# Kernel optimization log

Measured on AMD Instinct MI355X. Metric: run time of the kernel, lower is better.

The kernel has to match this reference:

```python
import jax, jax.numpy as jnp
import numpy as np

B, F, N_P, N_Q, DIM, H = 16, 16, 196, 32, 768, 12

def setup_inputs() -> dict:
    key = jax.random.key(0)
    ks = jax.random.split(key, 6)
    return {
        "x": jax.random.normal(ks[0], (B, F * N_P, DIM), jnp.float32),
        "question": jax.random.normal(ks[1], (B, N_Q, DIM), jnp.float32),
        "Wq": jax.random.normal(ks[2], (DIM, DIM), jnp.float32) * 0.02,
        "Wkv": jax.random.normal(ks[3], (DIM, 2 * DIM), jnp.float32) * 0.02,
        "Wproj": jax.random.normal(ks[4], (DIM, DIM), jnp.float32) * 0.02,
        "bproj": jnp.zeros((DIM,), jnp.float32),
        "mask": jnp.zeros((B, F * N_P), jnp.bool_),
        "whether": 0,
        "f": F,
    }

def reference(x, question, Wq, Wkv, Wproj, bproj, mask, whether, f):
    # mask and whether are unused by the original forward as well
    num_heads = H
    b, n_kv, dim = x.shape
    n_q = question.shape[1]
    d = dim // num_heads
    scale = d ** -0.5
    # projections; split heads: b n (h d) -> b h n d
    q = (question @ Wq).reshape(b, n_q, num_heads, d).transpose(0, 2, 1, 3) * scale
    k, v = jnp.split(x @ Wkv, 2, axis=-1)
    k = k.reshape(b, n_kv, num_heads, d).transpose(0, 2, 1, 3)
    v = v.reshape(b, n_kv, num_heads, d).transpose(0, 2, 1, 3)
    cls_q = q[:, :, :1]   # b h 1 d  -- CLS attends over all video tokens
    q_ = q[:, :, 1:]      # b h (n_q-1) d -- rest attend per-frame
    cls_sim = jnp.einsum('bhid,bhjd->bhij', cls_q, k)
    cls_out = jnp.einsum('bhij,bhjd->bhid', jax.nn.softmax(cls_sim, axis=-1), v)
    n_p = n_kv // f
    kf = k.reshape(b, num_heads, f, n_p, d)
    vf = v.reshape(b, num_heads, f, n_p, d)
    # q_ broadcast across frames == repeat_interleave(f, 0) in the original
    sim = jnp.einsum('bhid,bhfjd->bhfij', q_, kf)
    out = jnp.einsum('bhfij,bhfjd->bhfid', jax.nn.softmax(sim, axis=-1), vf)
    # '(b f) n d -> b (f n) d' with frame-major ordering
    out = out.reshape(b, num_heads, f * (n_q - 1), d)
    out = jnp.concatenate([cls_out, out], axis=2)  # b h (1 + f*(n_q-1)) d
    out = out.transpose(0, 2, 1, 3).reshape(b, 1 + f * (n_q - 1), dim)
    return out @ Wproj + bproj
```

## Files before the change

kernel.cpp:

```cpp
#include <hip/hip_runtime.h>

typedef unsigned short u16;
typedef __bf16 bf16x8 __attribute__((ext_vector_type(8)));
typedef float f32x4 __attribute__((ext_vector_type(4)));

__device__ __forceinline__ u16 f2bf(float f) {
  union { float f; unsigned u; } v; v.f = f;
  unsigned r = (v.u + 0x7FFFu + ((v.u >> 16) & 1u)) >> 16;
  return (u16)r;
}
__device__ __forceinline__ float bf2f(u16 u) {
  union { unsigned u; float f; } v; v.u = ((unsigned)u) << 16;
  return v.f;
}

#define GLD16(g, l) __builtin_amdgcn_global_load_lds((const __attribute__((address_space(1))) void*)(g), (__attribute__((address_space(3))) void*)(l), 16, 0, 0)
#define LOG2E 1.44269504f

__global__ __launch_bounds__(256) void mega_prep(const float* __restrict__ x, u16* __restrict__ xb,
                                                 int have_xb,
                                                 const float* __restrict__ Wq, u16* __restrict__ WqT,
                                                 const float* __restrict__ Wkv, u16* __restrict__ WkvT,
                                                 const float* __restrict__ Wproj, u16* __restrict__ WprojT) {
  __shared__ float t[32][33];
  int bid = blockIdx.x;
  if (bid < 2048) {
    if (!have_xb) return;
    const size_t n8 = (size_t)50176 * 768 / 8;
    const size_t stride = (size_t)2048 * 256;
    for (size_t i = (size_t)bid * 256 + threadIdx.x; i < n8; i += stride) {
      float4 a = *(const float4*)(x + i * 8);
      float4 b = *(const float4*)(x + i * 8 + 4);
      ushort4 oa, ob;
      oa.x = f2bf(a.x); oa.y = f2bf(a.y); oa.z = f2bf(a.z); oa.w = f2bf(a.w);
      ob.x = f2bf(b.x); ob.y = f2bf(b.y); ob.z = f2bf(b.z); ob.w = f2bf(b.w);
      ushort4* o = (ushort4*)(xb + i * 8);
      o[0] = oa; o[1] = ob;
    }
    return;
  }
  bid -= 2048;
  const float* in; u16* outp; int N;
  const int K = 768;
  if (bid < 576) { in = Wq; outp = WqT; N = 768; }
  else if (bid < 1728) { in = Wkv; outp = WkvT; N = 1536; bid -= 576; }
  else { in = Wproj; outp = WprojT; N = 768; bid -= 1728; }
  int nb = N >> 5;
  int bn = bid % nb, bk = bid / nb;
  int tx = threadIdx.x & 31, ty = threadIdx.x >> 5;
#pragma unroll
  for (int i = 0; i < 4; ++i)
    t[ty + i * 8][tx] = in[(size_t)(bk * 32 + ty + i * 8) * N + bn * 32 + tx];
  __syncthreads();
#pragma unroll
  for (int i = 0; i < 4; ++i)
    outp[(size_t)(bn * 32 + ty + i * 8) * K + bk * 32 + tx] = f2bf(t[tx][ty + i * 8]);
}

__global__ __launch_bounds__(512, 2) void gemm256_bt(const u16* __restrict__ A,
                                                     const u16* __restrict__ Bt,
                                                     u16* __restrict__ C,
                                                     int M, int N) {
  __shared__ __align__(16) char smem[131072];
  const int KB = 1536;
  int nb = N >> 8;
  int nwg = gridDim.x;
  int bid = blockIdx.x;
  if (!(nwg & 7)) { int cpx = nwg >> 3; bid = (bid & 7) * cpx + (bid >> 3); }
  int bm = bid / nb, bn = bid - bm * nb;
  int tid = threadIdx.x, lane = tid & 63, wid = tid >> 6;
  int wm = wid >> 2, wn = wid & 3;
  int l15 = lane & 15, g4 = lane >> 4;

  int goff[4][2], loff[4][2];
#pragma unroll
  for (int p = 0; p < 4; ++p) {
#pragma unroll
    for (int i = 0; i < 2; ++i) {
      int idx = wid * 2 + i;
      int ht = p & 1;
      int base;
      if (p < 2) base = ht * 8192 + (idx >> 3) * 16384 + (idx & 7) * 1024;
      else       base = (idx >> 2) * 8192 + ht * 4096 + (idx & 3) * 1024;
      int pb = base + 16 * lane;
      int lb = pb ^ (((pb >> 9) & 1) << 5);
      goff[p][i] = (lb >> 7) * KB + (lb & 127);
      loff[p][i] = pb;
    }
  }
  const char* Agb = (const char*)A + (size_t)bm * 256 * KB;
  const char* Bgb = (const char*)Bt + (size_t)bn * 256 * KB;

  auto STAGE = [&](int pat, int buf, int k0) {
    const char* gb = (pat < 2) ? Agb : Bgb;
    int lbase = buf * 65536 + ((pat < 2) ? 0 : 32768);
#pragma unroll
    for (int i = 0; i < 2; ++i)
      GLD16(gb + goff[pat][i] + k0 * 2, smem + lbase + loff[pat][i]);
  };

  f32x4 acc[8][4];
  const f32x4 fz = {0.f, 0.f, 0.f, 0.f};
#pragma unroll
  for (int a = 0; a < 8; ++a)
#pragma unroll
    for (int b = 0; b < 4; ++b) acc[a][b] = fz;
  bf16x8 af[4][2], bv[2][2];

  auto RDA = [&](int buf, int qm) {
#pragma unroll
    for (int mi = 0; mi < 4; ++mi)
#pragma unroll
      for (int ks = 0; ks < 2; ++ks) {
        int lb = (wm * 128 + qm * 64 + mi * 16 + l15) * 128 + ks * 64 + g4 * 16;
        int pb = lb ^ (((lb >> 9) & 1) << 5);
        af[mi][ks] = *(const bf16x8*)(smem + buf * 65536 + pb);
      }
  };
  auto RDB = [&](int buf, int qn) {
#pragma unroll
    for (int ni = 0; ni < 2; ++ni)
#pragma unroll
      for (int ks = 0; ks < 2; ++ks) {
        int lb = (wn * 64 + qn * 32 + ni * 16 + l15) * 128 + ks * 64 + g4 * 16;
        int pb = lb ^ (((lb >> 9) & 1) << 5);
        bv[ni][ks] = *(const bf16x8*)(smem + buf * 65536 + 32768 + pb);
      }
  };
  auto MM = [&](int qm, int qn) {
    __builtin_amdgcn_s_setprio(1);
#pragma unroll
    for (int mi = 0; mi < 4; ++mi)
#pragma unroll
      for (int ni = 0; ni < 2; ++ni)
#pragma unroll
        for (int ks = 0; ks < 2; ++ks)
          acc[qm * 4 + mi][qn * 2 + ni] =
              __builtin_amdgcn_mfma_f32_16x16x32_bf16(af[mi][ks], bv[ni][ks],
                                                      acc[qm * 4 + mi][qn * 2 + ni], 0, 0, 0);
    __builtin_amdgcn_s_setprio(0);
  };
#define BAR() __builtin_amdgcn_s_barrier()
#define LGKM0() asm volatile("s_waitcnt lgkmcnt(0)" ::: "memory")

  STAGE(0, 0, 0); STAGE(2, 0, 0); STAGE(1, 0, 0); STAGE(3, 0, 0);
  STAGE(0, 1, 64); STAGE(2, 1, 64);
  asm volatile("s_waitcnt vmcnt(4)" ::: "memory");
  BAR();

  for (int t = 0; t < 6; ++t) {
    int kO = t * 128 + 64, kE2 = t * 128 + 128, kO2 = t * 128 + 192;
    bool lst = (t == 5);
    RDA(0, 0); RDB(0, 0); STAGE(1, 1, kO);
    BAR(); LGKM0(); MM(0, 0); BAR();
    RDB(0, 1); STAGE(3, 1, kO);
    BAR(); LGKM0(); MM(0, 1); BAR();
    RDA(0, 1); RDB(0, 0); if (!lst) STAGE(0, 0, kE2);
    BAR(); LGKM0(); MM(1, 0); BAR();
    RDB(0, 1); if (!lst) STAGE(2, 0, kE2);
    BAR(); LGKM0(); MM(1, 1);
    if (lst) asm volatile("s_waitcnt vmcnt(0)" ::: "memory");
    else     asm volatile("s_waitcnt vmcnt(4)" ::: "memory");
    BAR();
    RDA(1, 0); RDB(1, 0); if (!lst) STAGE(1, 0, kE2);
    BAR(); LGKM0(); MM(0, 0); BAR();
    RDB(1, 1); if (!lst) STAGE(3, 0, kE2);
    BAR(); LGKM0(); MM(0, 1); BAR();
    RDA(1, 1); RDB(1, 0); if (!lst) STAGE(0, 1, kO2);
    BAR(); LGKM0(); MM(1, 0); BAR();
    RDB(1, 1); if (!lst) STAGE(2, 1, kO2);
    BAR(); LGKM0(); MM(1, 1);
    if (!lst) asm volatile("s_waitcnt vmcnt(4)" ::: "memory");
    BAR();
  }
#undef BAR
#undef LGKM0

#pragma unroll
  for (int a = 0; a < 8; ++a)
#pragma unroll
    for (int b = 0; b < 4; ++b)
#pragma unroll
      for (int r = 0; r < 4; ++r)
        C[(size_t)(bm * 256 + wm * 128 + a * 16 + g4 * 4 + r) * N + bn * 256 + wn * 64 + b * 16 + l15] =
            f2bf(acc[a][b][r]);
}

template <int AF32, int OUTF32>
__global__ __launch_bounds__(256) void gemm_bt(const void* __restrict__ Av,
                                               const u16* __restrict__ Bt,
                                               void* __restrict__ Cv,
                                               const float* __restrict__ bias,
                                               float scale, int M, int N, int K) {
  __shared__ u16 As[128 * 32];
  __shared__ u16 Bs[128 * 32];
  int nb = N >> 7;
  int nwg = gridDim.x;
  int bid = blockIdx.x;
  if (!(nwg & 7)) { int cpx = nwg >> 3; bid = (bid & 7) * cpx + (bid >> 3); }
  int bm = bid / nb, bn = bid - bm * nb;
  int tid = threadIdx.x, lane = tid & 63, w = tid >> 6;
  int wr = w >> 1, wc = w & 1;
  int l15 = lane & 15, g4 = lane >> 4;

  const f32x4 fz = {0.f, 0.f, 0.f, 0.f};
  f32x4 acc[4][4];
#pragma unroll
  for (int m = 0; m < 4; ++m)
#pragma unroll
    for (int n = 0; n < 4; ++n) acc[m][n] = fz;

  const int kIters = K >> 5;
  for (int kt = 0; kt < kIters; ++kt) {
    __syncthreads();
    const int k0 = kt << 5;
    if constexpr (AF32) {
      const float* Af = (const float*)Av;
#pragma unroll
      for (int i = 0; i < 4; ++i) {
        int c = tid + (i << 8);
        int row = c >> 3, cp = c & 7;
        int grow = bm * 128 + row; if (grow > M - 1) grow = M - 1;
        float4 v = *(const float4*)(Af + (size_t)grow * K + k0 + cp * 4);
        ushort4 o; o.x = f2bf(v.x); o.y = f2bf(v.y); o.z = f2bf(v.z); o.w = f2bf(v.w);
        *(ushort4*)&As[row * 32 + cp * 4] = o;
      }
    } else {
      const u16* Ab = (const u16*)Av;
#pragma unroll
      for (int i = 0; i < 2; ++i) {
        int c = tid + (i << 8);
        int row = c >> 2, cp = c & 3;
        int grow = bm * 128 + row; if (grow > M - 1) grow = M - 1;
        GLD16(Ab + (size_t)grow * K + k0 + cp * 8, &As[row * 32 + cp * 8]);
      }
    }
#pragma unroll
    for (int i = 0; i < 2; ++i) {
      int c = tid + (i << 8);
      int row = c >> 2, cp = c & 3;
      GLD16(Bt + (size_t)(bn * 128 + row) * K + k0 + cp * 8, &Bs[row * 32 + cp * 8]);
    }
    __syncthreads();
    bf16x8 af[4], bfr[4];
#pragma unroll
    for (int m = 0; m < 4; ++m)
      af[m] = *(const bf16x8*)&As[(wr * 64 + m * 16 + l15) * 32 + g4 * 8];
#pragma unroll
    for (int n = 0; n < 4; ++n)
      bfr[n] = *(const bf16x8*)&Bs[(wc * 64 + n * 16 + l15) * 32 + g4 * 8];
#pragma unroll
    for (int m = 0; m < 4; ++m)
#pragma unroll
      for (int n = 0; n < 4; ++n)
        acc[m][n] = __builtin_amdgcn_mfma_f32_16x16x32_bf16(af[m], bfr[n], acc[m][n], 0, 0, 0);
  }
  int r0 = bm * 128 + wr * 64;
  int c0 = bn * 128 + wc * 64;
#pragma unroll
  for (int m = 0; m < 4; ++m) {
#pragma unroll
    for (int n = 0; n < 4; ++n) {
      int col = c0 + n * 16 + l15;
      float badd = bias ? bias[col] : 0.f;
#pragma unroll
      for (int r = 0; r < 4; ++r) {
        int grow = r0 + m * 16 + g4 * 4 + r;
        if (grow < M) {
          float v = acc[m][n][r] * scale + badd;
          if constexpr (OUTF32) ((float*)Cv)[(size_t)grow * N + col] = v;
          else ((u16*)Cv)[(size_t)grow * N + col] = f2bf(v);
        }
      }
    }
  }
}

#define CLS_CH 16
__global__ __launch_bounds__(64) void cls_reduce(const float* __restrict__ part,
                                                 u16* __restrict__ ATT) {
  int bh = blockIdx.x;
  int b = bh / 12, h = bh % 12;
  int d = threadIdx.x;
  float m[CLS_CH], l[CLS_CH];
  float M = -1e30f;
#pragma unroll
  for (int c = 0; c < CLS_CH; ++c) {
    m[c] = part[(size_t)(bh * CLS_CH + c) * 66 + 64];
    l[c] = part[(size_t)(bh * CLS_CH + c) * 66 + 65];
    M = fmaxf(M, m[c]);
  }
  float L = 0.f, o = 0.f;
#pragma unroll
  for (int c = 0; c < CLS_CH; ++c) {
    float wgt = exp2f((m[c] - M) * LOG2E) * l[c];
    L += wgt;
    o += wgt * part[(size_t)(bh * CLS_CH + c) * 66 + d];
  }
  ATT[(size_t)(b * 497) * 768 + h * 64 + d] = f2bf(o / L);
}

#define VSTR 232
__global__ __launch_bounds__(256, 3) void frame_attn(const u16* __restrict__ Qp,
                                                     const u16* __restrict__ KV,
                                                     u16* __restrict__ ATT,
                                                     float* __restrict__ part) {
  __shared__ u16 Vt[64 * VSTR];
  __shared__ u16 P[32 * VSTR];
  __shared__ float redm[2][32];
  __shared__ float reds[2][32];

  int bid = blockIdx.x;
  int b = bid / 192;
  int h = (bid / 16) % 12;
  int f = bid % 16;
  int tid = threadIdx.x, lane = tid & 63, w = tid >> 6;
  int l15 = lane & 15, g4 = lane >> 4;
  int mt = w >> 1, nh = w & 1;

  const u16* Kb = KV + ((size_t)(b * 3136 + f * 196)) * 1536 + h * 64;
  const u16* Vb = Kb + 768;
  const u16* Qbp = Qp + (size_t)(b * 32) * 768 + h * 64;

  int qrow = mt * 16 + l15;
  bf16x8 qf[2];
  qf[0] = *(const bf16x8*)(Qbp + (size_t)qrow * 768 + g4 * 8);
  qf[1] = *(const bf16x8*)(Qbp + (size_t)qrow * 768 + 32 + g4 * 8);

  bf16x8 kfa[7][2];
#pragma unroll
  for (int nt = 0; nt < 7; ++nt) {
    if (!(nh == 1 && nt == 6)) {
      int j = nh * 112 + nt * 16 + l15;
      kfa[nt][0] = *(const bf16x8*)(Kb + (size_t)j * 1536 + g4 * 8);
      kfa[nt][1] = *(const bf16x8*)(Kb + (size_t)j * 1536 + 32 + g4 * 8);
    }
  }

  int vd8 = tid & 7;
  int vr0 = (tid >> 3) * 2;
  uint4 va[3][2];
#pragma unroll
  for (int i = 0; i < 3; ++i) {
    int j = vr0 + i * 64;
    va[i][0] = *(const uint4*)(Vb + (size_t)j * 1536 + vd8 * 8);
    va[i][1] = *(const uint4*)(Vb + (size_t)(j + 1) * 1536 + vd8 * 8);
  }
  bool vtail = (vr0 < 4);
  uint4 vt0, vt1;
  if (vtail) {
    vt0 = *(const uint4*)(Vb + (size_t)(vr0 + 192) * 1536 + vd8 * 8);
    vt1 = *(const uint4*)(Vb + (size_t)(vr0 + 193) * 1536 + vd8 * 8);
  }
  for (int c = tid; c < 64 * 28; c += 256) {
    int d = c / 28, j = 196 + (c - d * 28);
    Vt[d * VSTR + j] = 0;
  }

  const f32x4 fz = {0.f, 0.f, 0.f, 0.f};
  f32x4 s[7];
#pragma unroll
  for (int i = 0; i < 7; ++i) s[i] = fz;
#pragma unroll
  for (int nt = 0; nt < 7; ++nt) {
    if (!(nh == 1 && nt == 6)) {
      s[nt] = __builtin_amdgcn_mfma_f32_16x16x32_bf16(qf[0], kfa[nt][0], s[nt], 0, 0, 0);
      s[nt] = __builtin_amdgcn_mfma_f32_16x16x32_bf16(qf[1], kfa[nt][1], s[nt], 0, 0, 0);
    }
  }
  const f32x4 fneg = {-1e30f, -1e30f, -1e30f, -1e30f};
#pragma unroll
  for (int nt = 0; nt < 7; ++nt) {
    int j = nh * 112 + nt * 16 + l15;
    if (j >= 196) s[nt] = fneg;
  }
  float pm[4], psum[4];
#pragma unroll
  for (int r = 0; r < 4; ++r) {
    float m = s[0][r];
#pragma unroll
    for (int nt = 1; nt < 7; ++nt) m = fmaxf(m, s[nt][r]);
    m = fmaxf(m, __shfl_xor(m, 1));
    m = fmaxf(m, __shfl_xor(m, 2));
    m = fmaxf(m, __shfl_xor(m, 4));
    m = fmaxf(m, __shfl_xor(m, 8));
    pm[r] = m;
    psum[r] = 0.f;
  }
#pragma unroll
  for (int nt = 0; nt < 7; ++nt)
#pragma unroll
    for (int r = 0; r < 4; ++r) {
      float e = exp2f((s[nt][r] - pm[r]) * LOG2E);
      s[nt][r] = e;
      psum[r] += e;
    }
#pragma unroll
  for (int r = 0; r < 4; ++r) {
    psum[r] += __shfl_xor(psum[r], 1);
    psum[r] += __shfl_xor(psum[r], 2);
    psum[r] += __shfl_xor(psum[r], 4);
    psum[r] += __shfl_xor(psum[r], 8);
  }
  if (l15 == 0) {
#pragma unroll
    for (int r = 0; r < 4; ++r) {
      redm[nh][mt * 16 + g4 * 4 + r] = pm[r];
      reds[nh][mt * 16 + g4 * 4 + r] = psum[r];
    }
  }
  __syncthreads();

#pragma unroll
  for (int i = 0; i < 3; ++i) {
    const u16* a = (const u16*)&va[i][0];
    const u16* bq = (const u16*)&va[i][1];
    int j = vr0 + i * 64;
#pragma unroll
    for (int e = 0; e < 8; ++e) {
      unsigned wv = (unsigned)a[e] | ((unsigned)bq[e] << 16);
      *(unsigned*)&Vt[(vd8 * 8 + e) * VSTR + j] = wv;
    }
  }
  if (vtail) {
    const u16* a = (const u16*)&vt0;
    const u16* bq = (const u16*)&vt1;
    int j = vr0 + 192;
#pragma unroll
    for (int e = 0; e < 8; ++e) {
      unsigned wv = (unsigned)a[e] | ((unsigned)bq[e] << 16);
      *(unsigned*)&Vt[(vd8 * 8 + e) * VSTR + j] = wv;
    }
  }

  float M0 = 0.f, L0 = 1.f;
#pragma unroll
  for (int r = 0; r < 4; ++r) {
    int row = mt * 16 + g4 * 4 + r;
    float m0 = redm[0][row], m1 = redm[1][row];
    float M = fmaxf(m0, m1);
    float L = reds[0][row] * exp2f((m0 - M) * LOG2E) + reds[1][row] * exp2f((m1 - M) * LOG2E);
    if (r == 0) { M0 = M; L0 = L; }
    float fac = exp2f((pm[r] - M) * LOG2E) / L;
#pragma unroll
    for (int nt = 0; nt < 7; ++nt)
      P[row * VSTR + nh * 112 + nt * 16 + l15] = f2bf(s[nt][r] * fac);
  }
  __syncthreads();

  f32x4 o0 = fz, o1 = fz;
  int prow = mt * 16 + l15;
#pragma unroll
  for (int ks = 0; ks < 7; ++ks) {
    bf16x8 pa = *(const bf16x8*)&P[prow * VSTR + ks * 32 + g4 * 8];
    bf16x8 v0 = *(const bf16x8*)&Vt[(nh * 32 + l15) * VSTR + ks * 32 + g4 * 8];
    bf16x8 v1 = *(const bf16x8*)&Vt[(nh * 32 + 16 + l15) * VSTR + ks * 32 + g4 * 8];
    o0 = __builtin_amdgcn_mfma_f32_16x16x32_bf16(pa, v0, o0, 0, 0, 0);
    o1 = __builtin_amdgcn_mfma_f32_16x16x32_bf16(pa, v1, o1, 0, 0, 0);
  }
  u16* Ab = ATT + ((size_t)b * 497) * 768 + h * 64;
#pragma unroll
  for (int r = 0; r < 4; ++r) {
    int qi = mt * 16 + g4 * 4 + r;
    if (qi > 0) {
      size_t ro = (size_t)(f * 31 + qi) * 768;
      Ab[ro + nh * 32 + l15] = f2bf(o0[r]);
      Ab[ro + nh * 32 + 16 + l15] = f2bf(o1[r]);
    }
  }
  if (mt == 0 && g4 == 0) {
    float* po = part + (size_t)(((b * 12 + h) * 16) + f) * 66;
    po[nh * 32 + l15] = o0[0];
    po[nh * 32 + 16 + l15] = o1[0];
    if (nh == 0 && l15 == 0) { po[64] = M0; po[65] = L0; }
  }
}

extern "C" void kernel_launch(void* const* d_in, const int* in_sizes, int n_in,
                              void* d_out, int out_size, void* d_ws, size_t ws_size,
                              hipStream_t stream) {
  const float* x = (const float*)d_in[0];
  const float* question = (const float*)d_in[1];
  const float* Wq = (const float*)d_in[2];
  const float* Wkv = (const float*)d_in[3];
  const float* Wproj = (const float*)d_in[4];
  const float* bproj = (const float*)d_in[5];
  float* out = (float*)d_out;

  char* ws = (char*)d_ws;
  size_t off = 0;
  auto carve = [&](size_t elems) {
    u16* p = (u16*)(ws + off);
    off += ((elems * 2 + 255) & ~(size_t)255);
    return p;
  };
  u16* WqT = carve((size_t)768 * 768);
  u16* WkvT = carve((size_t)1536 * 768);
  u16* WprojT = carve((size_t)768 * 768);
  u16* Qb = carve((size_t)512 * 768);
  u16* KV = carve((size_t)50176 * 1536);
  u16* ATT = carve((size_t)7952 * 768);
  float* PART = (float*)carve((size_t)192 * CLS_CH * 66 * 2);
  size_t base_need = off;
  u16* xb = carve((size_t)50176 * 768);
  if (ws_size < base_need) return;
  int have_xb = (ws_size >= off) ? 1 : 0;

  mega_prep<<<2048 + 576 + 1152 + 576, 256, 0, stream>>>(x, xb, have_xb,
                                                         Wq, WqT, Wkv, WkvT, Wproj, WprojT);
  gemm_bt<1, 0><<<4 * 6, 256, 0, stream>>>(question, WqT, Qb, nullptr, 0.125f, 512, 768, 768);
  if (have_xb) {
    gemm256_bt<<<196 * 6, 512, 0, stream>>>(xb, WkvT, KV, 50176, 1536);
  } else {
    gemm_bt<1, 0><<<392 * 12, 256, 0, stream>>>(x, WkvT, KV, nullptr, 1.0f, 50176, 1536, 768);
  }
  frame_attn<<<3072, 256, 0, stream>>>(Qb, KV, ATT, PART);
  cls_reduce<<<192, 64, 0, stream>>>(PART, ATT);
  gemm_bt<0, 1><<<63 * 6, 256, 0, stream>>>(ATT, WprojT, out, bproj, 1.0f, 7952, 768, 768);
}
```

Baseline: 305.1 us.

## Fuse fp32-to-bf16 conversion of x into the KV projection GEMM

```diff
diff --git a/kernel.cpp b/kernel.cpp
--- a/kernel.cpp
+++ b/kernel.cpp
@@ -17,29 +17,11 @@
 #define GLD16(g, l) __builtin_amdgcn_global_load_lds((const __attribute__((address_space(1))) void*)(g), (__attribute__((address_space(3))) void*)(l), 16, 0, 0)
 #define LOG2E 1.44269504f
 
-__global__ __launch_bounds__(256) void mega_prep(const float* __restrict__ x, u16* __restrict__ xb,
-                                                 int have_xb,
-                                                 const float* __restrict__ Wq, u16* __restrict__ WqT,
+__global__ __launch_bounds__(256) void mega_prep(const float* __restrict__ Wq, u16* __restrict__ WqT,
                                                  const float* __restrict__ Wkv, u16* __restrict__ WkvT,
                                                  const float* __restrict__ Wproj, u16* __restrict__ WprojT) {
   __shared__ float t[32][33];
   int bid = blockIdx.x;
-  if (bid < 2048) {
-    if (!have_xb) return;
-    const size_t n8 = (size_t)50176 * 768 / 8;
-    const size_t stride = (size_t)2048 * 256;
-    for (size_t i = (size_t)bid * 256 + threadIdx.x; i < n8; i += stride) {
-      float4 a = *(const float4*)(x + i * 8);
-      float4 b = *(const float4*)(x + i * 8 + 4);
-      ushort4 oa, ob;
-      oa.x = f2bf(a.x); oa.y = f2bf(a.y); oa.z = f2bf(a.z); oa.w = f2bf(a.w);
-      ob.x = f2bf(b.x); ob.y = f2bf(b.y); ob.z = f2bf(b.z); ob.w = f2bf(b.w);
-      ushort4* o = (ushort4*)(xb + i * 8);
-      o[0] = oa; o[1] = ob;
-    }
-    return;
-  }
-  bid -= 2048;
   const float* in; u16* outp; int N;
   const int K = 768;
   if (bid < 576) { in = Wq; outp = WqT; N = 768; }
@@ -57,11 +39,12 @@
     outp[(size_t)(bn * 32 + ty + i * 8) * K + bk * 32 + tx] = f2bf(t[tx][ty + i * 8]);
 }
 
-__global__ __launch_bounds__(512, 2) void gemm256_bt(const u16* __restrict__ A,
+__global__ __launch_bounds__(512, 2) void gemm256_ax(const float* __restrict__ Af,
                                                      const u16* __restrict__ Bt,
                                                      u16* __restrict__ C,
                                                      int M, int N) {
   __shared__ __align__(16) char smem[131072];
+  const int KBf = 3072;
   const int KB = 1536;
   int nb = N >> 8;
   int nwg = gridDim.x;
@@ -72,7 +55,7 @@
   int wm = wid >> 2, wn = wid & 3;
   int l15 = lane & 15, g4 = lane >> 4;
 
-  int goff[4][2], loff[4][2];
+  int ga32[2][2], gb[2][2], loffA[2][2], loffB[2][2];
 #pragma unroll
   for (int p = 0; p < 4; ++p) {
 #pragma unroll
@@ -84,19 +67,41 @@
       else       base = (idx >> 2) * 8192 + ht * 4096 + (idx & 3) * 1024;
       int pb = base + 16 * lane;
       int lb = pb ^ (((pb >> 9) & 1) << 5);
-      goff[p][i] = (lb >> 7) * KB + (lb & 127);
-      loff[p][i] = pb;
-    }
-  }
-  const char* Agb = (const char*)A + (size_t)bm * 256 * KB;
+      if (p < 2) { ga32[p][i] = (lb >> 7) * KBf + (lb & 127) * 2; loffA[p][i] = pb; }
+      else       { gb[p - 2][i] = (lb >> 7) * KB + (lb & 127);    loffB[p - 2][i] = pb; }
+    }
+  }
+  const char* Agb = (const char*)Af + (size_t)bm * 256 * KBf;
   const char* Bgb = (const char*)Bt + (size_t)bn * 256 * KB;
 
-  auto STAGE = [&](int pat, int buf, int k0) {
-    const char* gb = (pat < 2) ? Agb : Bgb;
-    int lbase = buf * 65536 + ((pat < 2) ? 0 : 32768);
+  float4 ar[2][2];
+  auto LDA = [&](int pat, int k0) {
+#pragma unroll
+    for (int i = 0; i < 2; ++i) {
+      const char* s = Agb + ga32[pat][i] + k0 * 4;
+      ar[i][0] = *(const float4*)(s);
+      ar[i][1] = *(const float4*)(s + 16);
+    }
+  };
+  auto WRA = [&](int pat, int buf) {
+#pragma unroll
+    for (int i = 0; i < 2; ++i) {
+      union { u16 h[8]; uint4 v; } r;
+      const float* f0 = (const float*)&ar[i][0];
+      const float* f1 = (const float*)&ar[i][1];
+#pragma unroll
+      for (int e = 0; e < 4; ++e) {
+        union { __bf16 b; u16 u; } c0; c0.b = (__bf16)f0[e]; r.h[e] = c0.u;
+        union { __bf16 b; u16 u; } c1; c1.b = (__bf16)f1[e]; r.h[4 + e] = c1.u;
+      }
+      *(uint4*)(smem + buf * 65536 + loffA[pat][i]) = r.v;
+    }
+  };
+  auto SB = [&](int pat, int buf, int k0) {
+    int lbase = buf * 65536 + 32768;
 #pragma unroll
     for (int i = 0; i < 2; ++i)
-      GLD16(gb + goff[pat][i] + k0 * 2, smem + lbase + loff[pat][i]);
+      GLD16(Bgb + gb[pat][i] + k0 * 2, smem + lbase + loffB[pat][i]);
   };
 
   f32x4 acc[8][4];
@@ -142,39 +147,48 @@
   };
 #define BAR() __builtin_amdgcn_s_barrier()
 #define LGKM0() asm volatile("s_waitcnt lgkmcnt(0)" ::: "memory")
-
-  STAGE(0, 0, 0); STAGE(2, 0, 0); STAGE(1, 0, 0); STAGE(3, 0, 0);
-  STAGE(0, 1, 64); STAGE(2, 1, 64);
-  asm volatile("s_waitcnt vmcnt(4)" ::: "memory");
+#define VMC(n) asm volatile("s_waitcnt vmcnt(" #n ")" ::: "memory")
+
+  SB(0, 0, 0); SB(1, 0, 0);
+  LDA(0, 0);
+  VMC(0);
+  WRA(0, 0);
+  LDA(1, 0);
+  VMC(0);
+  WRA(1, 0);
+  LDA(0, 64);
+  SB(0, 1, 64);
+  LGKM0();
   BAR();
 
   for (int t = 0; t < 6; ++t) {
     int kO = t * 128 + 64, kE2 = t * 128 + 128, kO2 = t * 128 + 192;
     bool lst = (t == 5);
-    RDA(0, 0); RDB(0, 0); STAGE(1, 1, kO);
+    VMC(2); WRA(0, 1);  RDA(0, 0); RDB(0, 0); LDA(1, kO);
     BAR(); LGKM0(); MM(0, 0); BAR();
-    RDB(0, 1); STAGE(3, 1, kO);
+    RDB(0, 1); SB(1, 1, kO);
     BAR(); LGKM0(); MM(0, 1); BAR();
-    RDA(0, 1); RDB(0, 0); if (!lst) STAGE(0, 0, kE2);
+    VMC(2); WRA(1, 1);  RDA(0, 1); RDB(0, 0); if (!lst) LDA(0, kE2);
     BAR(); LGKM0(); MM(1, 0); BAR();
-    RDB(0, 1); if (!lst) STAGE(2, 0, kE2);
+    RDB(0, 1); if (!lst) SB(0, 0, kE2);
     BAR(); LGKM0(); MM(1, 1);
-    if (lst) asm volatile("s_waitcnt vmcnt(0)" ::: "memory");
-    else     asm volatile("s_waitcnt vmcnt(4)" ::: "memory");
+    if (lst) VMC(0); else VMC(6);
     BAR();
-    RDA(1, 0); RDB(1, 0); if (!lst) STAGE(1, 0, kE2);
+    if (!lst) { VMC(2); WRA(0, 0); }  RDA(1, 0); RDB(1, 0); if (!lst) LDA(1, kE2);
     BAR(); LGKM0(); MM(0, 0); BAR();
-    RDB(1, 1); if (!lst) STAGE(3, 0, kE2);
+    RDB(1, 1); if (!lst) SB(1, 0, kE2);
     BAR(); LGKM0(); MM(0, 1); BAR();
-    RDA(1, 1); RDB(1, 0); if (!lst) STAGE(0, 1, kO2);
+    if (!lst) { VMC(2); WRA(1, 0); RDA(1, 1); RDB(1, 0); LDA(0, kO2); }
+    else      { RDA(1, 1); RDB(1, 0); }
     BAR(); LGKM0(); MM(1, 0); BAR();
-    RDB(1, 1); if (!lst) STAGE(2, 1, kO2);
+    RDB(1, 1); if (!lst) SB(0, 1, kO2);
     BAR(); LGKM0(); MM(1, 1);
-    if (!lst) asm volatile("s_waitcnt vmcnt(4)" ::: "memory");
+    if (!lst) VMC(6);
     BAR();
   }
 #undef BAR
 #undef LGKM0
+#undef VMC
 
 #pragma unroll
   for (int a = 0; a < 8; ++a)
@@ -501,19 +515,11 @@
   u16* KV = carve((size_t)50176 * 1536);
   u16* ATT = carve((size_t)7952 * 768);
   float* PART = (float*)carve((size_t)192 * CLS_CH * 66 * 2);
-  size_t base_need = off;
-  u16* xb = carve((size_t)50176 * 768);
-  if (ws_size < base_need) return;
-  int have_xb = (ws_size >= off) ? 1 : 0;
-
-  mega_prep<<<2048 + 576 + 1152 + 576, 256, 0, stream>>>(x, xb, have_xb,
-                                                         Wq, WqT, Wkv, WkvT, Wproj, WprojT);
+  if (ws_size < off) return;
+
+  mega_prep<<<576 + 1152 + 576, 256, 0, stream>>>(Wq, WqT, Wkv, WkvT, Wproj, WprojT);
   gemm_bt<1, 0><<<4 * 6, 256, 0, stream>>>(question, WqT, Qb, nullptr, 0.125f, 512, 768, 768);
-  if (have_xb) {
-    gemm256_bt<<<196 * 6, 512, 0, stream>>>(xb, WkvT, KV, 50176, 1536);
-  } else {
-    gemm_bt<1, 0><<<392 * 12, 256, 0, stream>>>(x, WkvT, KV, nullptr, 1.0f, 50176, 1536, 768);
-  }
+  gemm256_ax<<<196 * 6, 512, 0, stream>>>(x, WkvT, KV, 50176, 1536);
   frame_attn<<<3072, 256, 0, stream>>>(Qb, KV, ATT, PART);
   cls_reduce<<<192, 64, 0, stream>>>(PART, ATT);
   gemm_bt<0, 1><<<63 * 6, 256, 0, stream>>>(ATT, WprojT, out, bproj, 1.0f, 7952, 768, 768);
```

Result: slower. 443.3 us (+45.3%).
